# Optimization experiments

Measured on AMD Instinct MI355X. Metric: run time of the kernel, lower is better.

Reference implementation:

```python
import jax, jax.numpy as jnp
import numpy as np

EPSILON = 1e-8
K = 3
PAD = K // 2


def setup_inputs() -> dict:
    key = jax.random.key(0)
    k1, k2, k3, k4 = jax.random.split(key, 4)
    B, FI, FO, H, W, DSTYLE = 8, 512, 512, 64, 64, 512
    return {
        "x": jax.random.normal(k1, (B, FI, H, W), dtype=jnp.float32),
        "style": jax.random.normal(k2, (B, DSTYLE), dtype=jnp.float32),
        "w": jax.random.normal(k3, (FO, FI, K, K), dtype=jnp.float32),
        "fc_w": jax.random.normal(k4, (FI, DSTYLE), dtype=jnp.float32),  # modLinear weight [dim_out=fi, dim_in=dim_style]
        "fc_b": jnp.zeros((FI,), dtype=jnp.float32),
    }


def reference(x, style, w, fc_w, fc_b):
    B, FI, H, W = x.shape
    FO = w.shape[0]
    DSTYLE = fc_w.shape[1]
    fc_scale = DSTYLE ** (-0.5)            # modLinear w_scale (lr_mult=1)
    w_scale = (FI * K * K) ** (-0.5)       # modConv w_scale

    # modLinear: style -> per-input-channel modulation s, shape [B, FI]
    s = style @ (fc_w * fc_scale).T + fc_b

    # Demod factor: d[b, fo] = rsqrt(sum_{fi,k,k} (w_scale * w * s[b,fi])^2 + eps)
    wsq = jnp.sum((w * w_scale) ** 2, axis=(2, 3))          # [FO, FI]
    d = jax.lax.rsqrt(jnp.einsum('of,bf->bo', wsq, s ** 2) + EPSILON)  # [B, FO]

    # Equivalent to per-sample grouped conv: scale input channels by s,
    # conv with shared base weight, scale output channels by demod.
    xm = x * s[:, :, None, None]
    y = jax.lax.conv_general_dilated(
        xm, w * w_scale,
        window_strides=(1, 1),
        padding=((PAD, PAD), (PAD, PAD)),
        dimension_numbers=('NCHW', 'OIHW', 'NCHW'),
    )
    return y * d[:, :, None, None]
```

## Files before the change

kernel.cpp:

```cpp
#include <hip/hip_runtime.h>


typedef __bf16 bf16_t;
typedef __bf16 bf16x8 __attribute__((ext_vector_type(8)));
typedef float floatx4 __attribute__((ext_vector_type(4)));

#define HW_ 4096
#define FCSCALE 0.04419417382415922f
#define WSCALE  0.014731391274719742f

#define VMCNT(n) asm volatile("s_waitcnt vmcnt(" #n ")" ::: "memory")

__device__ __forceinline__ void gload_lds16(const bf16_t* g, bf16_t* l) {
  __builtin_amdgcn_global_load_lds(
      (const __attribute__((address_space(1))) void*)g,
      (__attribute__((address_space(3))) void*)l, 16, 0, 0);
}

__global__ void k_style(const float* __restrict__ style, const float* __restrict__ fc_w,
                        const float* __restrict__ fc_b, float* __restrict__ s_out) {
  int o = blockIdx.x * 4 + (threadIdx.x >> 6);
  int lane = threadIdx.x & 63;
  int b = o >> 9, fi = o & 511;
  const float4* st = (const float4*)(style + b * 512);
  const float4* fw = (const float4*)(fc_w + (size_t)fi * 512);
  float4 a0 = st[lane * 2],     w0 = fw[lane * 2];
  float4 a1 = st[lane * 2 + 1], w1 = fw[lane * 2 + 1];
  float acc = a0.x * w0.x + a0.y * w0.y + a0.z * w0.z + a0.w * w0.w
            + a1.x * w1.x + a1.y * w1.y + a1.z * w1.z + a1.w * w1.w;
#pragma unroll
  for (int d = 32; d >= 1; d >>= 1) acc += __shfl_xor(acc, d, 64);
  if (lane == 0) s_out[o] = acc * FCSCALE + fc_b[fi];
}

__global__ void k_wsq_wt(const float* __restrict__ w, float* __restrict__ wsq,
                         bf16_t* __restrict__ wt) {
  int idx = blockIdx.x * 256 + threadIdx.x;
  int fo = idx >> 9, fi = idx & 511;
  const float* wp = w + (size_t)idx * 9;
  float v[9], q = 0.f;
#pragma unroll
  for (int k = 0; k < 9; ++k) { v[k] = wp[k] * WSCALE; q += v[k] * v[k]; }
  wsq[idx] = q;
#pragma unroll
  for (int k = 0; k < 9; ++k)
    wt[((((size_t)k * 64) + (fi >> 3)) * 512 + fo) * 8 + (fi & 7)] = (bf16_t)v[k];
}

__global__ void k_demod(const float* __restrict__ wsq, const float* __restrict__ s,
                        float* __restrict__ dcoef) {
  int o = blockIdx.x * 4 + (threadIdx.x >> 6);
  int lane = threadIdx.x & 63;
  int b = o >> 9, fo = o & 511;
  const float4* wq = (const float4*)(wsq + (size_t)fo * 512);
  const float4* sp = (const float4*)(s + b * 512);
  float acc = 0.f;
#pragma unroll
  for (int i = 0; i < 2; ++i) {
    float4 q = wq[lane * 2 + i], sv = sp[lane * 2 + i];
    acc += q.x * sv.x * sv.x + q.y * sv.y * sv.y + q.z * sv.z * sv.z + q.w * sv.w * sv.w;
  }
#pragma unroll
  for (int d = 32; d >= 1; d >>= 1) acc += __shfl_xor(acc, d, 64);
  if (lane == 0) dcoef[o] = rsqrtf(acc + 1e-8f);
}

__global__ void k_modx(const float* __restrict__ x, const float* __restrict__ s,
                       bf16_t* __restrict__ xT) {
  __shared__ float tile[32][65];
  int b = blockIdx.z;
  int fi0 = blockIdx.x * 32;
  int h = blockIdx.y;
  int t = threadIdx.x;
  int c4 = (t & 15) * 4, fr = t >> 4;
#pragma unroll
  for (int i = 0; i < 2; ++i) {
    int fi_l = i * 16 + fr;
    float sv = s[b * 512 + fi0 + fi_l];
    float4 v = *(const float4*)(x + ((size_t)(b * 512 + fi0 + fi_l)) * HW_ + h * 64 + c4);
    tile[fi_l][c4] = v.x * sv; tile[fi_l][c4 + 1] = v.y * sv;
    tile[fi_l][c4 + 2] = v.z * sv; tile[fi_l][c4 + 3] = v.w * sv;
  }
  __syncthreads();
  int g_l = t >> 6, wcol = t & 63;
  bf16x8 vv;
#pragma unroll
  for (int j = 0; j < 8; ++j) vv[j] = (bf16_t)tile[g_l * 8 + j][wcol];
  *(bf16x8*)&xT[((((size_t)(b * 64 + h)) * 64 + (fi0 >> 3) + g_l) * 64 + wcol) * 8] = vv;
}

__global__ __launch_bounds__(256, 2) void k_conv(const bf16_t* __restrict__ wt,
                                                 const bf16_t* __restrict__ xT,
                                                 const float* __restrict__ dcoef,
                                                 const bf16_t* __restrict__ zerobuf,
                                                 float* __restrict__ out) {
  __shared__ __align__(16) bf16_t wls[4 * 4 * 128 * 8];

  int b   = blockIdx.x;
  int foB = blockIdx.y;
  int hq  = blockIdx.z;
  int t = threadIdx.x;
  int wv = t >> 6, lane = t & 63, quad = lane >> 4, l16 = lane & 15;
  int h0 = hq * 4;
  int fo_l = t & 127, chunk_hi = t >> 7;

  const bf16_t* xTb = xT + (size_t)b * 64 * 64 * 64 * 8;

  floatx4 acc[8][4];
#pragma unroll
  for (int i = 0; i < 8; ++i)
#pragma unroll
    for (int j = 0; j < 4; ++j) acc[i][j] = (floatx4){0.f, 0.f, 0.f, 0.f};

  auto stage_w = [&](int it, int pf) {
    int tap = it >> 4;
    int g0 = (it & 15) * 4;
#pragma unroll
    for (int itw = 0; itw < 2; ++itw) {
      int cw = itw * 2 + chunk_hi;
      gload_lds16(wt + ((((size_t)tap * 64) + g0 + cw) * 512 + foB * 128 + fo_l) * 8,
                  &wls[(size_t)pf * 4096 + (itw * 256 + wv * 64) * 8]);
    }
  };

  auto load_x = [&](int it, bf16x8* xf) {
    int tap = it >> 4;
    int g0 = (it & 15) * 4;
    int kh = tap / 3, kw = tap - kh * 3;
    int rg = h0 + wv + kh - 1;
    bool rok = (unsigned)rg < 64u;
    const bf16_t* rowp = xTb + (((size_t)rg * 64 + g0 + quad) * 64) * 8;
#pragma unroll
    for (int j = 0; j < 4; ++j) {
      int c = j * 16 + l16 + kw - 1;
      const bf16_t* src = (rok && (unsigned)c < 64u) ? rowp + (size_t)c * 8
                                                     : zerobuf;
      xf[j] = *(const bf16x8*)src;
    }
  };

  auto compute = [&](int pc, const bf16x8* xf) {
    const bf16_t* wb = &wls[(size_t)pc * 4096];
    __builtin_amdgcn_s_setprio(1);
#pragma unroll
    for (int i = 0; i < 8; ++i) {
      bf16x8 afr = *(const bf16x8*)&wb[(quad * 128 + i * 16 + l16) * 8];
#pragma unroll
      for (int j = 0; j < 4; ++j)
        acc[i][j] = __builtin_amdgcn_mfma_f32_16x16x32_bf16(afr, xf[j], acc[i][j], 0, 0, 0);
    }
    __builtin_amdgcn_s_setprio(0);
  };

  bf16x8 xfA[4], xfB[4];

  stage_w(0, 0);
  load_x(0, xfA);
  stage_w(1, 1);

  for (int it = 0; it < 140; it += 2) {
    load_x(it + 1, xfB);
    stage_w(it + 2, (it + 2) & 3);
    VMCNT(8);
    __builtin_amdgcn_s_barrier();
    __builtin_amdgcn_sched_barrier(0);
    compute(it & 3, xfA);
    load_x(it + 2, xfA);
    stage_w(it + 3, (it + 3) & 3);
    VMCNT(8);
    __builtin_amdgcn_s_barrier();
    __builtin_amdgcn_sched_barrier(0);
    compute((it + 1) & 3, xfB);
  }
  load_x(141, xfB);
  stage_w(142, 2);
  VMCNT(8);
  __builtin_amdgcn_s_barrier();
  __builtin_amdgcn_sched_barrier(0);
  compute(0, xfA);
  load_x(142, xfA);
  stage_w(143, 3);
  VMCNT(8);
  __builtin_amdgcn_s_barrier();
  __builtin_amdgcn_sched_barrier(0);
  compute(1, xfB);
  load_x(143, xfB);
  VMCNT(6);
  __builtin_amdgcn_s_barrier();
  __builtin_amdgcn_sched_barrier(0);
  compute(2, xfA);
  VMCNT(0);
  __builtin_amdgcn_s_barrier();
  __builtin_amdgcn_sched_barrier(0);
  compute(3, xfB);

  int h = h0 + wv;
#pragma unroll
  for (int i = 0; i < 8; ++i) {
#pragma unroll
    for (int rr = 0; rr < 4; ++rr) {
      int fo_g = foB * 128 + i * 16 + quad * 4 + rr;
      float dm = dcoef[b * 512 + fo_g];
      float* op = out + ((size_t)((b * 512 + fo_g) * 64 + h)) * 64;
#pragma unroll
      for (int j = 0; j < 4; ++j)
        op[j * 16 + l16] = acc[i][j][rr] * dm;
    }
  }
}

extern "C" void kernel_launch(void* const* d_in, const int* in_sizes, int n_in,
                              void* d_out, int out_size, void* d_ws, size_t ws_size,
                              hipStream_t stream) {
  const float* x     = (const float*)d_in[0];
  const float* style = (const float*)d_in[1];
  const float* w     = (const float*)d_in[2];
  const float* fc_w  = (const float*)d_in[3];
  const float* fc_b  = (const float*)d_in[4];
  float* out = (float*)d_out;
  char* ws = (char*)d_ws;

  float*  s       = (float*)(ws);
  float*  dcoef   = (float*)(ws + 16384);
  float*  wsq     = (float*)(ws + 32768);
  bf16_t* zerobuf = (bf16_t*)(ws + 1081344);
  bf16_t* wt      = (bf16_t*)(ws + 1081600);
  bf16_t* xT      = (bf16_t*)(ws + 5800192);

  hipMemsetAsync(zerobuf, 0, 256, stream);
  k_style<<<1024, 256, 0, stream>>>(style, fc_w, fc_b, s);
  k_wsq_wt<<<1024, 256, 0, stream>>>(w, wsq, wt);
  k_demod<<<1024, 256, 0, stream>>>(wsq, s, dcoef);
  k_modx<<<dim3(16, 64, 8), 256, 0, stream>>>(x, s, xT);
  k_conv<<<dim3(8, 4, 16), 256, 0, stream>>>(wt, xT, dcoef, zerobuf, out);
}
```

Measured before the change: 277.9 us.

## Merge prep kernels into two launches and reorder conv K-loop tap-innermost

```diff
diff --git a/kernel.cpp b/kernel.cpp
--- a/kernel.cpp
+++ b/kernel.cpp
@@ -17,10 +17,12 @@
       (__attribute__((address_space(3))) void*)l, 16, 0, 0);
 }
 
-__global__ void k_style(const float* __restrict__ style, const float* __restrict__ fc_w,
-                        const float* __restrict__ fc_b, float* __restrict__ s_out) {
-  int o = blockIdx.x * 4 + (threadIdx.x >> 6);
-  int lane = threadIdx.x & 63;
+
+__device__ __forceinline__ void style_body(int bid, int t,
+    const float* __restrict__ style, const float* __restrict__ fc_w,
+    const float* __restrict__ fc_b, float* __restrict__ s_out) {
+  int o = bid * 4 + (t >> 6);
+  int lane = t & 63;
   int b = o >> 9, fi = o & 511;
   const float4* st = (const float4*)(style + b * 512);
   const float4* fw = (const float4*)(fc_w + (size_t)fi * 512);
@@ -33,9 +35,9 @@
   if (lane == 0) s_out[o] = acc * FCSCALE + fc_b[fi];
 }
 
-__global__ void k_wsq_wt(const float* __restrict__ w, float* __restrict__ wsq,
-                         bf16_t* __restrict__ wt) {
-  int idx = blockIdx.x * 256 + threadIdx.x;
+__device__ __forceinline__ void wsq_wt_body(int bid, int t,
+    const float* __restrict__ w, float* __restrict__ wsq, bf16_t* __restrict__ wt) {
+  int idx = bid * 256 + t;
   int fo = idx >> 9, fi = idx & 511;
   const float* wp = w + (size_t)idx * 9;
   float v[9], q = 0.f;
@@ -47,10 +49,11 @@
     wt[((((size_t)k * 64) + (fi >> 3)) * 512 + fo) * 8 + (fi & 7)] = (bf16_t)v[k];
 }
 
-__global__ void k_demod(const float* __restrict__ wsq, const float* __restrict__ s,
-                        float* __restrict__ dcoef) {
-  int o = blockIdx.x * 4 + (threadIdx.x >> 6);
-  int lane = threadIdx.x & 63;
+__device__ __forceinline__ void demod_body(int bid, int t,
+    const float* __restrict__ wsq, const float* __restrict__ s,
+    float* __restrict__ dcoef) {
+  int o = bid * 4 + (t >> 6);
+  int lane = t & 63;
   int b = o >> 9, fo = o & 511;
   const float4* wq = (const float4*)(wsq + (size_t)fo * 512);
   const float4* sp = (const float4*)(s + b * 512);
@@ -65,13 +68,23 @@
   if (lane == 0) dcoef[o] = rsqrtf(acc + 1e-8f);
 }
 
-__global__ void k_modx(const float* __restrict__ x, const float* __restrict__ s,
-                       bf16_t* __restrict__ xT) {
-  __shared__ float tile[32][65];
-  int b = blockIdx.z;
-  int fi0 = blockIdx.x * 32;
-  int h = blockIdx.y;
-  int t = threadIdx.x;
+__global__ void k_prep1(const float* __restrict__ style, const float* __restrict__ fc_w,
+                        const float* __restrict__ fc_b, const float* __restrict__ w,
+                        float* __restrict__ s_out, float* __restrict__ wsq,
+                        bf16_t* __restrict__ wt, bf16_t* __restrict__ zerobuf) {
+  int blk = blockIdx.x, t = threadIdx.x;
+  if (blk < 1024) {
+    wsq_wt_body(blk, t, w, wsq, wt);
+  } else if (blk < 2048) {
+    style_body(blk - 1024, t, style, fc_w, fc_b, s_out);
+  } else {
+    if (t < 128) zerobuf[t] = (bf16_t)0.f;
+  }
+}
+
+__device__ __forceinline__ void modx_body(int fi0, int h, int b, int t,
+    const float* __restrict__ x, const float* __restrict__ s,
+    bf16_t* __restrict__ xT, float (*tile)[65]) {
   int c4 = (t & 15) * 4, fr = t >> 4;
 #pragma unroll
   for (int i = 0; i < 2; ++i) {
@@ -87,6 +100,21 @@
 #pragma unroll
   for (int j = 0; j < 8; ++j) vv[j] = (bf16_t)tile[g_l * 8 + j][wcol];
   *(bf16x8*)&xT[((((size_t)(b * 64 + h)) * 64 + (fi0 >> 3) + g_l) * 64 + wcol) * 8] = vv;
+}
+
+__global__ void k_prep2(const float* __restrict__ x, const float* __restrict__ s,
+                        const float* __restrict__ wsq, float* __restrict__ dcoef,
+                        bf16_t* __restrict__ xT) {
+  __shared__ float tile[32][65];
+  int blk = blockIdx.x, t = threadIdx.x;
+  if (blk < 1024) {
+    demod_body(blk, t, wsq, s, dcoef);
+  } else {
+    int m = blk - 1024;
+    int b = m >> 10, rem = m & 1023;
+    int h = rem >> 4, fi0 = (rem & 15) * 32;
+    modx_body(fi0, h, b, t, x, s, xT, tile);
+  }
 }
 
 __global__ __launch_bounds__(256, 2) void k_conv(const bf16_t* __restrict__ wt,
@@ -113,8 +141,9 @@
     for (int j = 0; j < 4; ++j) acc[i][j] = (floatx4){0.f, 0.f, 0.f, 0.f};
 
   auto stage_w = [&](int it, int pf) {
-    int tap = it >> 4;
-    int g0 = (it & 15) * 4;
+    int gc = (it * 7282) >> 16;
+    int tap = it - gc * 9;
+    int g0 = gc * 4;
 #pragma unroll
     for (int itw = 0; itw < 2; ++itw) {
       int cw = itw * 2 + chunk_hi;
@@ -124,8 +153,9 @@
   };
 
   auto load_x = [&](int it, bf16x8* xf) {
-    int tap = it >> 4;
-    int g0 = (it & 15) * 4;
+    int gc = (it * 7282) >> 16;
+    int tap = it - gc * 9;
+    int g0 = gc * 4;
     int kh = tap / 3, kw = tap - kh * 3;
     int rg = h0 + wv + kh - 1;
     bool rok = (unsigned)rg < 64u;
@@ -227,10 +257,7 @@
   bf16_t* wt      = (bf16_t*)(ws + 1081600);
   bf16_t* xT      = (bf16_t*)(ws + 5800192);
 
-  hipMemsetAsync(zerobuf, 0, 256, stream);
-  k_style<<<1024, 256, 0, stream>>>(style, fc_w, fc_b, s);
-  k_wsq_wt<<<1024, 256, 0, stream>>>(w, wsq, wt);
-  k_demod<<<1024, 256, 0, stream>>>(wsq, s, dcoef);
-  k_modx<<<dim3(16, 64, 8), 256, 0, stream>>>(x, s, xT);
+  k_prep1<<<2049, 256, 0, stream>>>(style, fc_w, fc_b, w, s, wsq, wt, zerobuf);
+  k_prep2<<<9216, 256, 0, stream>>>(x, s, wsq, dcoef, xT);
   k_conv<<<dim3(8, 4, 16), 256, 0, stream>>>(wt, xT, dcoef, zerobuf, out);
 }
```

After: 253.2 us. -8.9%, faster.
